# Kernel tuning notes

Measured on AMD Instinct MI355X. Metric: run time of the kernel, lower is better.

The kernel has to match this reference:

```python
import jax, jax.numpy as jnp
import numpy as np

D_MODEL, D_HEAD, N_HEAD, PERIOD = 1024, 64, 16, 30
B, T1, T2 = 2, 2048, 2048


def setup_inputs() -> dict:
    key = jax.random.key(0)
    ks = jax.random.split(key, 7)
    s_in = 1.0 / np.sqrt(D_MODEL)
    s_out = 1.0 / np.sqrt(N_HEAD * D_HEAD)
    return {
        "x": jax.random.normal(ks[0], (B, T1, D_MODEL), dtype=jnp.float32),
        "context": jax.random.normal(ks[1], (B, T2, D_MODEL), dtype=jnp.float32),
        "Wq": jax.random.uniform(ks[2], (N_HEAD * D_HEAD, D_MODEL), jnp.float32, -s_in, s_in),
        "Wk": jax.random.uniform(ks[3], (N_HEAD * D_HEAD, D_MODEL), jnp.float32, -s_in, s_in),
        "Wv": jax.random.uniform(ks[4], (N_HEAD * D_HEAD, D_MODEL), jnp.float32, -s_in, s_in),
        "Wo": jax.random.uniform(ks[5], (D_MODEL, N_HEAD * D_HEAD), jnp.float32, -s_out, s_out),
        "bo": jax.random.uniform(ks[6], (D_MODEL,), jnp.float32, -s_out, s_out),
    }


def reference(x, context, Wq, Wk, Wv, Wo, bo):
    Bx, T1x, _ = x.shape
    T2x = context.shape[1]
    scale = 1.0 / np.sqrt(D_HEAD).astype(np.float32)
    # projections (torch Linear: y = x @ W^T)
    q = (x @ Wq.T).reshape(Bx, T1x, N_HEAD, D_HEAD)
    k = (context @ Wk.T).reshape(Bx, T2x, N_HEAD, D_HEAD)
    v = (context @ Wv.T).reshape(Bx, T2x, N_HEAD, D_HEAD)
    # attention scores [B, H, T1, T2]
    scores = jnp.einsum('bihd,bjhd->bhij', q, k) * scale
    # ALiBi-style periodic distance bias
    dist = jnp.abs(jnp.arange(T1x)[:, None] - jnp.arange(T2x)[None, :])  # [T1,T2]
    bias = -(dist // PERIOD).astype(jnp.float32)                          # [T1,T2]
    head_scale = jnp.power(2.0, -jnp.arange(1, N_HEAD + 1, dtype=jnp.float32))
    biased = scores + bias[None, None, :, :] * head_scale[None, :, None, None]
    attn = jax.nn.softmax(biased, axis=-1)
    out = jnp.einsum('bhij,bjhd->bihd', attn, v).reshape(Bx, T1x, N_HEAD * D_HEAD)
    # output projection; dropout is identity in eval mode
    return out @ Wo.T + bo
```

## Files before the change

kernel.cpp:

```cpp
#include <hip/hip_runtime.h>
#include <hip/hip_fp16.h>

typedef _Float16 f16;
typedef __attribute__((ext_vector_type(8))) _Float16 f16x8;
typedef __attribute__((ext_vector_type(4))) _Float16 f16x4;
typedef __attribute__((ext_vector_type(2))) __fp16 fp16x2;
typedef __attribute__((ext_vector_type(4))) float f32x4;
typedef __attribute__((ext_vector_type(16))) float f32x16;

#define DM 1024
#define NH 16
#define DH 64
#define TT 2048
#define LOG2E 1.4426950408889634f
#define QSCALE 0.18033688f

__device__ __forceinline__ void gl16(const void* g, void* l) {
  __builtin_amdgcn_global_load_lds((const __attribute__((address_space(1))) void*)g,
                                   (__attribute__((address_space(3))) void*)l, 16, 0, 0);
}

#define SB0 __builtin_amdgcn_sched_barrier(0)

__global__ __launch_bounds__(256) void cvt_all(const float* __restrict__ x, const float* __restrict__ cx,
                                               const float* __restrict__ wq, const float* __restrict__ wk,
                                               const float* __restrict__ wv, const float* __restrict__ wo,
                                               f16* __restrict__ xb, f16* __restrict__ cb,
                                               f16* __restrict__ wqb, f16* __restrict__ wkb,
                                               f16* __restrict__ wvb, f16* __restrict__ wob,
                                               f16* __restrict__ FBf) {
  int idx = blockIdx.x * 256 + threadIdx.x;
  int stride = gridDim.x * 256;
  for (int i = idx; i < 3670016; i += stride) {
    if (i >= 3145728) {
      int c = i - 3145728;
      int half = c & 1, lane = (c >> 1) & 63, kvt = (c >> 7) & 63, qt = c >> 13;
      int qi = qt * 32 + (lane & 31);
      int jb = kvt * 32 + 16 * half + 8 * (lane >> 5);
      f16x8 v;
#pragma unroll
      for (int e = 0; e < 8; e++) {
        int d = qi - (jb + e); d = (d < 0) ? -d : d;
        v[e] = (f16)(d / 30);
      }
      reinterpret_cast<f16x8*>(FBf)[c] = v;
      continue;
    }
    const float* src; f16* dst; int off; float s = 1.0f;
    if (i < 2097152) {
      if (i < 1048576) { src = x; dst = xb; off = i; }
      else { src = cx; dst = cb; off = i - 1048576; }
    } else {
      int j = i - 2097152;
      int wsel = j >> 18;
      off = j & 262143;
      if (wsel == 0) { src = wq; dst = wqb; s = QSCALE; }
      else if (wsel == 1) { src = wk; dst = wkb; }
      else if (wsel == 2) { src = wv; dst = wvb; }
      else { src = wo; dst = wob; }
    }
    float4 v = reinterpret_cast<const float4*>(src)[off];
    f16x4 o = { (f16)(v.x * s), (f16)(v.y * s), (f16)(v.z * s), (f16)(v.w * s) };
    reinterpret_cast<f16x4*>(dst)[off] = o;
  }
}

__device__ __forceinline__ void gemm_mainloop(const f16* __restrict__ A, const f16* __restrict__ W,
                                              int bm, int bn, f16 (*As)[4096], f16 (*Bs)[4096],
                                              f32x4 (&acc)[4][4]) {
  int t = threadIdx.x;
  int w = t >> 6;
  int lane = t & 63, lr = lane & 15, g = lane >> 4;
  int wr = w >> 1, wc = w & 1;
  int scol = ((t & 3) ^ ((t >> 3) & 3)) * 8;
  const f16* a0 = A + (size_t)(bm + (t >> 2)) * DM + scol;
  const f16* b0 = W + (size_t)(bn + (t >> 2)) * DM + scol;
  int wo = w * 512;
  int szg = ((lr >> 1) & 3) << 4;

  auto STG = [&](int bufi, int kt) {
    gl16(a0 + kt, As[bufi] + wo);
    gl16(a0 + kt + (size_t)64 * DM, As[bufi] + 2048 + wo);
    gl16(b0 + kt, Bs[bufi] + wo);
    gl16(b0 + kt + (size_t)64 * DM, Bs[bufi] + 2048 + wo);
  };

  STG(0, 0);
  __syncthreads();
  int buf = 0;
  for (int kt = 0; kt < DM; kt += 32) {
    if (kt + 32 < DM) STG(buf ^ 1, kt + 32);
    const char* Ab = (const char*)As[buf];
    const char* Bb = (const char*)Bs[buf];
    f16x8 af[4], bf[4];
#pragma unroll
    for (int mi = 0; mi < 4; mi++) {
      int row = wr * 64 + mi * 16 + lr;
      af[mi] = *reinterpret_cast<const f16x8*>(Ab + row * 64 + ((g << 4) ^ szg));
    }
#pragma unroll
    for (int ni = 0; ni < 4; ni++) {
      int row = wc * 64 + ni * 16 + lr;
      bf[ni] = *reinterpret_cast<const f16x8*>(Bb + row * 64 + ((g << 4) ^ szg));
    }
    __builtin_amdgcn_s_setprio(1);
#pragma unroll
    for (int mi = 0; mi < 4; mi++)
#pragma unroll
      for (int ni = 0; ni < 4; ni++)
        acc[mi][ni] = __builtin_amdgcn_mfma_f32_16x16x32_f16(af[mi], bf[ni], acc[mi][ni], 0, 0, 0);
    __builtin_amdgcn_s_setprio(0);
    __syncthreads();
    buf ^= 1;
  }
}

__global__ __launch_bounds__(256) void qkv_gemm(const f16* __restrict__ xb, const f16* __restrict__ cb,
                                                const f16* __restrict__ wq, const f16* __restrict__ wk,
                                                const f16* __restrict__ wv,
                                                f16* __restrict__ Qo, f16* __restrict__ Ko,
                                                f16* __restrict__ Vt) {
  __shared__ f16 As[2][4096];
  __shared__ f16 Bs[2][4096];
  int gid = blockIdx.x >> 8;
  int bid = blockIdx.x & 255;
  int bm = (bid >> 3) * 128, bn = (bid & 7) * 128;
  const f16* A = (gid == 0) ? xb : cb;
  const f16* W = (gid == 0) ? wq : ((gid == 1) ? wk : wv);
  f32x4 acc[4][4] = {};
  gemm_mainloop(A, W, bm, bn, As, Bs, acc);

  int t = threadIdx.x, w = t >> 6, lane = t & 63, lr = lane & 15, g = lane >> 4;
  int wr = w >> 1, wc = w & 1;
  if (gid < 2) {
    f16* out = (gid == 0) ? Qo : Ko;
#pragma unroll
    for (int mi = 0; mi < 4; mi++) {
      int m0 = bm + wr * 64 + mi * 16 + 4 * g;
      int b = m0 >> 11, i0 = m0 & 2047;
#pragma unroll
      for (int ni = 0; ni < 4; ni++) {
        int n = bn + wc * 64 + ni * 16 + lr;
        int h = n >> 6, d = n & 63;
        size_t base = (((size_t)(b * NH + h)) * TT + i0) * DH + d;
#pragma unroll
        for (int r = 0; r < 4; r++)
          out[base + (size_t)r * DH] = (f16)acc[mi][ni][r];
      }
    }
  } else {
#pragma unroll
    for (int mi = 0; mi < 4; mi++) {
      int m0 = bm + wr * 64 + mi * 16 + 4 * g;
      int b = m0 >> 11, j0 = m0 & 2047;
#pragma unroll
      for (int ni = 0; ni < 4; ni++) {
        int n = bn + wc * 64 + ni * 16 + lr;
        int h = n >> 6, d = n & 63;
        f16x4 pk = { (f16)acc[mi][ni][0], (f16)acc[mi][ni][1],
                     (f16)acc[mi][ni][2], (f16)acc[mi][ni][3] };
        *reinterpret_cast<f16x4*>(&Vt[(((size_t)(b * NH + h)) * DH + d) * TT + j0]) = pk;
      }
    }
  }
}

__global__ __launch_bounds__(256) void out_gemm(const f16* __restrict__ Ob, const f16* __restrict__ wo,
                                                const float* __restrict__ bo, float* __restrict__ Y) {
  __shared__ f16 As[2][4096];
  __shared__ f16 Bs[2][4096];
  int bid = blockIdx.x;
  int bm = (bid >> 3) * 128, bn = (bid & 7) * 128;
  f32x4 acc[4][4] = {};
  gemm_mainloop(Ob, wo, bm, bn, As, Bs, acc);
  int t = threadIdx.x, w = t >> 6, lane = t & 63, lr = lane & 15, g = lane >> 4;
  int wr = w >> 1, wc = w & 1;
#pragma unroll
  for (int mi = 0; mi < 4; mi++) {
    int m0 = bm + wr * 64 + mi * 16 + 4 * g;
#pragma unroll
    for (int ni = 0; ni < 4; ni++) {
      int n = bn + wc * 64 + ni * 16 + lr;
      float bias = bo[n];
#pragma unroll
      for (int r = 0; r < 4; r++)
        Y[(size_t)(m0 + r) * DM + n] = acc[mi][ni][r] + bias;
    }
  }
}

__global__ __launch_bounds__(64, 2) void attn_kernel(const f16* __restrict__ Q, const f16* __restrict__ K,
                                                     const f16* __restrict__ V, const f16* __restrict__ FBf,
                                                     f16* __restrict__ O) {
  __shared__ f16 KV[2][4096];
  int o = blockIdx.x;
  int xcd = o & 7, idx = o >> 3;
  int bh = 4 * xcd + (idx >> 6), qt = idx & 63;
  int h = bh & 15, b = bh >> 4;
  int l = threadIdx.x;
  int col = l & 31, hi = l >> 5;
  int qi = qt * 32 + col;

  const f16* qp = Q + ((size_t)bh * TT + qi) * DH + hi * 8;
  f16x8 qf[4];
#pragma unroll
  for (int s = 0; s < 4; s++) qf[s] = *reinterpret_cast<const f16x8*>(qp + 16 * s);

  const float nc2 = -exp2f(-(float)(h + 1)) * LOG2E;
  const f16x8* fbp = reinterpret_cast<const f16x8*>(FBf) + ((size_t)qt << 13) + (l << 1);

  f32x4 rsv = { 0.f, 0.f, 0.f, 0.f };
  f32x16 oacc0 = {}, oacc1 = {};

  int r8 = l >> 3, G = l & 7;
  const f16 *kps[4], *vps[4];
#pragma unroll
  for (int c = 0; c < 4; c++) {
    int rho = c * 8 + r8;
    int g0k = G ^ (rho & 7);
    int J = (rho & 19) | ((rho & 4) << 1) | ((rho & 8) >> 1);
    kps[c] = K + ((size_t)bh * TT + J) * DH + g0k * 8;
    int pi = c * 8 + r8;
    int g0v = G ^ (pi & 7);
    int dv = 2 * pi + (g0v >> 2), jg = g0v & 3;
    vps[c] = V + ((size_t)bh * DH + dv) * TT + jg * 8;
  }

  auto STG = [&](int bufi, int kv0) {
    f16* base = KV[bufi];
#pragma unroll
    for (int c = 0; c < 4; c++) gl16(kps[c] + (size_t)kv0 * DH, base + c * 512);
#pragma unroll
    for (int c = 0; c < 4; c++) gl16(vps[c] + kv0, base + 2048 + c * 512);
  };

  int kbase = col * 128;
  int ksw[4];
#pragma unroll
  for (int s = 0; s < 4; s++) ksw[s] = ((2 * s + hi) ^ (col & 7)) << 4;
  int vbyte[2][2];
#pragma unroll
  for (int db = 0; db < 2; db++)
#pragma unroll
    for (int s2 = 0; s2 < 2; s2++) {
      int pi = 16 * db + (col >> 1);
      int gl = (col & 1) * 4 + 2 * s2 + hi;
      vbyte[db][s2] = 4096 + pi * 128 + ((gl ^ (pi & 7)) << 4);
    }

  auto CMP = [&](int bufi, f16x8 fb0, f16x8 fb1) {
    const char* Kb = (const char*)KV[bufi];
    f32x16 S = {};
    __builtin_amdgcn_s_setprio(1);
#pragma unroll
    for (int s = 0; s < 4; s++) {
      f16x8 ka = *reinterpret_cast<const f16x8*>(Kb + kbase + ksw[s]);
      S = __builtin_amdgcn_mfma_f32_32x32x16_f16(ka, qf[s], S, 0, 0, 0);
    }
    __builtin_amdgcn_s_setprio(0);
    float p[16];
#pragma unroll
    for (int r = 0; r < 16; r++) {
      float fbf = (float)((r < 8) ? fb0[r] : fb1[r - 8]);
      p[r] = __builtin_amdgcn_exp2f(fmaf(fbf, nc2, S[r]));
    }
#pragma unroll
    for (int r = 0; r < 4; r++) {
      f32x4 pv = { p[4 * r], p[4 * r + 1], p[4 * r + 2], p[4 * r + 3] };
      rsv += pv;
    }
    f16x8 pb[2];
#pragma unroll
    for (int s2 = 0; s2 < 2; s2++) {
      union { f16x8 v; fp16x2 hh[4]; } pu;
#pragma unroll
      for (int q2 = 0; q2 < 4; q2++)
        pu.hh[q2] = __builtin_amdgcn_cvt_pkrtz(p[8 * s2 + 2 * q2], p[8 * s2 + 2 * q2 + 1]);
      pb[s2] = pu.v;
    }
    __builtin_amdgcn_s_setprio(1);
#pragma unroll
    for (int s2 = 0; s2 < 2; s2++) {
      f16x8 va0 = *reinterpret_cast<const f16x8*>(Kb + vbyte[0][s2]);
      f16x8 va1 = *reinterpret_cast<const f16x8*>(Kb + vbyte[1][s2]);
      oacc0 = __builtin_amdgcn_mfma_f32_32x32x16_f16(va0, pb[s2], oacc0, 0, 0, 0);
      oacc1 = __builtin_amdgcn_mfma_f32_32x32x16_f16(va1, pb[s2], oacc1, 0, 0, 0);
    }
    __builtin_amdgcn_s_setprio(0);
  };

  STG(0, 0);
  f16x8 fA0 = fbp[0], fA1 = fbp[1];
  f16x8 fB0, fB1;

  for (int kvt = 0; kvt < 64; kvt += 2) {
    SB0;
    STG(1, (kvt + 1) << 5);
    fB0 = fbp[(kvt + 1) * 128];
    fB1 = fbp[(kvt + 1) * 128 + 1];
    asm volatile("s_waitcnt vmcnt(10)" ::: "memory");
    SB0;
    CMP(0, fA0, fA1);
    SB0;
    if (kvt + 2 < 64) {
      STG(0, (kvt + 2) << 5);
      fA0 = fbp[(kvt + 2) * 128];
      fA1 = fbp[(kvt + 2) * 128 + 1];
      asm volatile("s_waitcnt vmcnt(10)" ::: "memory");
    } else {
      asm volatile("s_waitcnt vmcnt(0)" ::: "memory");
    }
    SB0;
    CMP(1, fB0, fB1);
  }

  float lsum = (rsv[0] + rsv[1]) + (rsv[2] + rsv[3]);
  lsum += __shfl_xor(lsum, 32, 64);
  float inv = __builtin_amdgcn_rcpf(lsum);

  size_t ob = ((size_t)b * TT + qi) * DM + h * DH + 4 * hi;
  const f32x16* oa[2] = { &oacc0, &oacc1 };
#pragma unroll
  for (int db = 0; db < 2; db++)
#pragma unroll
    for (int a = 0; a < 4; a++) {
      f16x4 o4 = { (f16)((*oa[db])[4 * a] * inv),     (f16)((*oa[db])[4 * a + 1] * inv),
                   (f16)((*oa[db])[4 * a + 2] * inv), (f16)((*oa[db])[4 * a + 3] * inv) };
      *reinterpret_cast<f16x4*>(&O[ob + 32 * db + 8 * a]) = o4;
    }
}

extern "C" void kernel_launch(void* const* d_in, const int* in_sizes, int n_in,
                              void* d_out, int out_size, void* d_ws, size_t ws_size,
                              hipStream_t stream) {
  const float* x  = (const float*)d_in[0];
  const float* cx = (const float*)d_in[1];
  const float* Wq = (const float*)d_in[2];
  const float* Wk = (const float*)d_in[3];
  const float* Wv = (const float*)d_in[4];
  const float* Wo = (const float*)d_in[5];
  const float* bo = (const float*)d_in[6];
  float* Y = (float*)d_out;

  const size_t NTOK = (size_t)2 * TT;
  f16* p = (f16*)d_ws;
  f16* xb  = p; p += NTOK * DM;
  f16* cb  = p; p += NTOK * DM;
  f16* wqb = p; p += (size_t)DM * DM;
  f16* wkb = p; p += (size_t)DM * DM;
  f16* wvb = p; p += (size_t)DM * DM;
  f16* wob = p; p += (size_t)DM * DM;
  f16* Qb  = p; p += NTOK * DM;
  f16* Kb  = p; p += NTOK * DM;
  f16* Vtb = p; p += NTOK * DM;
  f16* Ob  = p; p += NTOK * DM;
  f16* FBt = p;

  cvt_all<<<2048, 256, 0, stream>>>(x, cx, Wq, Wk, Wv, Wo, xb, cb, wqb, wkb, wvb, wob, FBt);
  qkv_gemm<<<768, 256, 0, stream>>>(xb, cb, wqb, wkb, wvb, Qb, Kb, Vtb);
  attn_kernel<<<2048, 64, 0, stream>>>(Qb, Kb, Vtb, FBt, Ob);
  out_gemm<<<256, 256, 0, stream>>>(Ob, wob, bo, Y);
}
```

Baseline: 144.1 us.

## Share K/V tiles across four waves per block with register-staged double buffering

The attention kernel moves from one 64-thread wave per 32 queries to a 256-thread block of four waves covering 128 queries. The four waves share each K/V tile staged in LDS, and each tile is now 64 keys instead of 32. Staging changes from direct global-to-LDS loads to register loads followed by LDS writes, with block barriers between buffers. This cuts redundant K/V global traffic by a factor of four, at the cost of barrier synchronisation and higher register pressure from doubled score tiles.

```diff
diff --git a/kernel.cpp b/kernel.cpp
--- a/kernel.cpp
+++ b/kernel.cpp
@@ -21,6 +21,7 @@
 }
 
 #define SB0 __builtin_amdgcn_sched_barrier(0)
+#define LGKM0 asm volatile("s_waitcnt lgkmcnt(0)" ::: "memory")
 
 __global__ __launch_bounds__(256) void cvt_all(const float* __restrict__ x, const float* __restrict__ cx,
                                                const float* __restrict__ wq, const float* __restrict__ wk,
@@ -189,17 +190,19 @@
   }
 }
 
-__global__ __launch_bounds__(64, 2) void attn_kernel(const f16* __restrict__ Q, const f16* __restrict__ K,
-                                                     const f16* __restrict__ V, const f16* __restrict__ FBf,
-                                                     f16* __restrict__ O) {
-  __shared__ f16 KV[2][4096];
+struct FB4 { f16x8 a, b, c, d; };
+
+__global__ __launch_bounds__(256, 2) void attn_kernel(const f16* __restrict__ Q, const f16* __restrict__ K,
+                                                      const f16* __restrict__ V, const f16* __restrict__ FBf,
+                                                      f16* __restrict__ O) {
+  __shared__ f16 KV[2][8192];
   int o = blockIdx.x;
   int xcd = o & 7, idx = o >> 3;
-  int bh = 4 * xcd + (idx >> 6), qt = idx & 63;
+  int bh = 4 * xcd + (idx >> 4), qblk = idx & 15;
   int h = bh & 15, b = bh >> 4;
-  int l = threadIdx.x;
-  int col = l & 31, hi = l >> 5;
-  int qi = qt * 32 + col;
+  int tt = threadIdx.x, w = tt >> 6, lane = tt & 63;
+  int col = lane & 31, hi = lane >> 5;
+  int qi = qblk * 128 + w * 32 + col;
 
   const f16* qp = Q + ((size_t)bh * TT + qi) * DH + hi * 8;
   f16x8 qf[4];
@@ -207,111 +210,124 @@
   for (int s = 0; s < 4; s++) qf[s] = *reinterpret_cast<const f16x8*>(qp + 16 * s);
 
   const float nc2 = -exp2f(-(float)(h + 1)) * LOG2E;
-  const f16x8* fbp = reinterpret_cast<const f16x8*>(FBf) + ((size_t)qt << 13) + (l << 1);
+  int qtp = qblk * 4 + w;
+  const f16x8* fbp = reinterpret_cast<const f16x8*>(FBf) + ((size_t)qtp << 13) + (lane << 1);
 
   f32x4 rsv = { 0.f, 0.f, 0.f, 0.f };
   f32x16 oacc0 = {}, oacc1 = {};
 
-  int r8 = l >> 3, G = l & 7;
-  const f16 *kps[4], *vps[4];
-#pragma unroll
-  for (int c = 0; c < 4; c++) {
-    int rho = c * 8 + r8;
-    int g0k = G ^ (rho & 7);
-    int J = (rho & 19) | ((rho & 4) << 1) | ((rho & 8) >> 1);
-    kps[c] = K + ((size_t)bh * TT + J) * DH + g0k * 8;
-    int pi = c * 8 + r8;
-    int g0v = G ^ (pi & 7);
-    int dv = 2 * pi + (g0v >> 2), jg = g0v & 3;
-    vps[c] = V + ((size_t)bh * DH + dv) * TT + jg * 8;
-  }
-
-  auto STG = [&](int bufi, int kv0) {
-    f16* base = KV[bufi];
-#pragma unroll
-    for (int c = 0; c < 4; c++) gl16(kps[c] + (size_t)kv0 * DH, base + c * 512);
-#pragma unroll
-    for (int c = 0; c < 4; c++) gl16(vps[c] + kv0, base + 2048 + c * 512);
-  };
-
-  int kbase = col * 128;
+  int rho0 = tt >> 3, G = tt & 7;
+  int f0 = (rho0 & 7) ^ (3 * ((rho0 >> 4) & 1));
+  int J0 = (rho0 & 19) | ((rho0 & 4) << 1) | ((rho0 & 8) >> 1);
+  const f16* kp0 = K + ((size_t)bh * TT + J0) * DH + (G ^ f0) * 8;
+  const f16* kp1 = K + ((size_t)bh * TT + 32 + J0) * DH + (G ^ f0) * 8;
+  const f16* vp0 = V + ((size_t)bh * DH + rho0) * TT + (G ^ f0) * 8;
+  const f16* vp1 = V + ((size_t)bh * DH + 32 + rho0) * TT + (G ^ f0) * 8;
+
+  f16x8 r0, r1, r2, r3;
+  auto LOADR = [&](int kv0) {
+    r0 = *reinterpret_cast<const f16x8*>(kp0 + (size_t)kv0 * DH);
+    r1 = *reinterpret_cast<const f16x8*>(kp1 + (size_t)kv0 * DH);
+    r2 = *reinterpret_cast<const f16x8*>(vp0 + kv0);
+    r3 = *reinterpret_cast<const f16x8*>(vp1 + kv0);
+  };
+  auto WRITE = [&](int bufi) {
+    char* base = (char*)KV[bufi];
+    *reinterpret_cast<f16x8*>(base + tt * 16) = r0;
+    *reinterpret_cast<f16x8*>(base + 4096 + tt * 16) = r1;
+    *reinterpret_cast<f16x8*>(base + 8192 + tt * 16) = r2;
+    *reinterpret_cast<f16x8*>(base + 12288 + tt * 16) = r3;
+  };
+
+  int fcol = (col & 7) ^ (3 * ((col >> 4) & 1));
+  int kb0 = col * 128;
   int ksw[4];
 #pragma unroll
-  for (int s = 0; s < 4; s++) ksw[s] = ((2 * s + hi) ^ (col & 7)) << 4;
-  int vbyte[2][2];
-#pragma unroll
-  for (int db = 0; db < 2; db++)
+  for (int s = 0; s < 4; s++) ksw[s] = ((2 * s + hi) ^ fcol) << 4;
+
+  auto FBLOAD = [&](int t) {
+    FB4 f;
+    f.a = fbp[256 * t];
+    f.b = fbp[256 * t + 1];
+    f.c = fbp[256 * t + 128];
+    f.d = fbp[256 * t + 129];
+    return f;
+  };
+
+  auto CMP = [&](int bufi, const FB4& fb) {
+    const char* Kb = (const char*)KV[bufi];
+    f32x16 S0 = {}, S1 = {};
+    __builtin_amdgcn_s_setprio(1);
+#pragma unroll
+    for (int s = 0; s < 4; s++) {
+      f16x8 ka0 = *reinterpret_cast<const f16x8*>(Kb + kb0 + ksw[s]);
+      f16x8 ka1 = *reinterpret_cast<const f16x8*>(Kb + 4096 + kb0 + ksw[s]);
+      S0 = __builtin_amdgcn_mfma_f32_32x32x16_f16(ka0, qf[s], S0, 0, 0, 0);
+      S1 = __builtin_amdgcn_mfma_f32_32x32x16_f16(ka1, qf[s], S1, 0, 0, 0);
+    }
+    __builtin_amdgcn_s_setprio(0);
+    float p0[16], p1[16];
+#pragma unroll
+    for (int r = 0; r < 16; r++) {
+      float fb0 = (float)((r < 8) ? fb.a[r] : fb.b[r - 8]);
+      float fb1 = (float)((r < 8) ? fb.c[r] : fb.d[r - 8]);
+      p0[r] = __builtin_amdgcn_exp2f(fmaf(fb0, nc2, S0[r]));
+      p1[r] = __builtin_amdgcn_exp2f(fmaf(fb1, nc2, S1[r]));
+    }
+#pragma unroll
+    for (int r = 0; r < 4; r++) {
+      f32x4 pa = { p0[4 * r], p0[4 * r + 1], p0[4 * r + 2], p0[4 * r + 3] };
+      f32x4 pc = { p1[4 * r], p1[4 * r + 1], p1[4 * r + 2], p1[4 * r + 3] };
+      rsv += pa + pc;
+    }
+    f16x8 pb[4];
 #pragma unroll
     for (int s2 = 0; s2 < 2; s2++) {
-      int pi = 16 * db + (col >> 1);
-      int gl = (col & 1) * 4 + 2 * s2 + hi;
-      vbyte[db][s2] = 4096 + pi * 128 + ((gl ^ (pi & 7)) << 4);
-    }
-
-  auto CMP = [&](int bufi, f16x8 fb0, f16x8 fb1) {
-    const char* Kb = (const char*)KV[bufi];
-    f32x16 S = {};
+      union { f16x8 v; fp16x2 hh[4]; } u0, u1;
+#pragma unroll
+      for (int q2 = 0; q2 < 4; q2++) {
+        u0.hh[q2] = __builtin_amdgcn_cvt_pkrtz(p0[8 * s2 + 2 * q2], p0[8 * s2 + 2 * q2 + 1]);
+        u1.hh[q2] = __builtin_amdgcn_cvt_pkrtz(p1[8 * s2 + 2 * q2], p1[8 * s2 + 2 * q2 + 1]);
+      }
+      pb[s2] = u0.v; pb[2 + s2] = u1.v;
+    }
     __builtin_amdgcn_s_setprio(1);
 #pragma unroll
-    for (int s = 0; s < 4; s++) {
-      f16x8 ka = *reinterpret_cast<const f16x8*>(Kb + kbase + ksw[s]);
-      S = __builtin_amdgcn_mfma_f32_32x32x16_f16(ka, qf[s], S, 0, 0, 0);
-    }
-    __builtin_amdgcn_s_setprio(0);
-    float p[16];
-#pragma unroll
-    for (int r = 0; r < 16; r++) {
-      float fbf = (float)((r < 8) ? fb0[r] : fb1[r - 8]);
-      p[r] = __builtin_amdgcn_exp2f(fmaf(fbf, nc2, S[r]));
-    }
-#pragma unroll
-    for (int r = 0; r < 4; r++) {
-      f32x4 pv = { p[4 * r], p[4 * r + 1], p[4 * r + 2], p[4 * r + 3] };
-      rsv += pv;
-    }
-    f16x8 pb[2];
-#pragma unroll
-    for (int s2 = 0; s2 < 2; s2++) {
-      union { f16x8 v; fp16x2 hh[4]; } pu;
-#pragma unroll
-      for (int q2 = 0; q2 < 4; q2++)
-        pu.hh[q2] = __builtin_amdgcn_cvt_pkrtz(p[8 * s2 + 2 * q2], p[8 * s2 + 2 * q2 + 1]);
-      pb[s2] = pu.v;
-    }
-    __builtin_amdgcn_s_setprio(1);
-#pragma unroll
-    for (int s2 = 0; s2 < 2; s2++) {
-      f16x8 va0 = *reinterpret_cast<const f16x8*>(Kb + vbyte[0][s2]);
-      f16x8 va1 = *reinterpret_cast<const f16x8*>(Kb + vbyte[1][s2]);
+    for (int s2 = 0; s2 < 4; s2++) {
+      f16x8 va0 = *reinterpret_cast<const f16x8*>(Kb + 8192 + kb0 + ksw[s2]);
+      f16x8 va1 = *reinterpret_cast<const f16x8*>(Kb + 12288 + kb0 + ksw[s2]);
       oacc0 = __builtin_amdgcn_mfma_f32_32x32x16_f16(va0, pb[s2], oacc0, 0, 0, 0);
       oacc1 = __builtin_amdgcn_mfma_f32_32x32x16_f16(va1, pb[s2], oacc1, 0, 0, 0);
     }
     __builtin_amdgcn_s_setprio(0);
   };
 
-  STG(0, 0);
-  f16x8 fA0 = fbp[0], fA1 = fbp[1];
-  f16x8 fB0, fB1;
-
-  for (int kvt = 0; kvt < 64; kvt += 2) {
+  LOADR(0);
+  WRITE(0);
+  LOADR(64);
+  FB4 fA = FBLOAD(0);
+  FB4 fB = FBLOAD(1);
+  LGKM0;
+  __builtin_amdgcn_s_barrier();
+  SB0;
+
+#pragma unroll 1
+  for (int tp = 0; tp < 16; tp++) {
+    int t0 = 2 * tp;
+    CMP(0, fA);
+    WRITE(1);
+    if (t0 + 2 < 32) { LOADR((t0 + 2) << 6); fA = FBLOAD(t0 + 2); }
+    LGKM0;
+    __builtin_amdgcn_s_barrier();
     SB0;
-    STG(1, (kvt + 1) << 5);
-    fB0 = fbp[(kvt + 1) * 128];
-    fB1 = fbp[(kvt + 1) * 128 + 1];
-    asm volatile("s_waitcnt vmcnt(10)" ::: "memory");
-    SB0;
-    CMP(0, fA0, fA1);
-    SB0;
-    if (kvt + 2 < 64) {
-      STG(0, (kvt + 2) << 5);
-      fA0 = fbp[(kvt + 2) * 128];
-      fA1 = fbp[(kvt + 2) * 128 + 1];
-      asm volatile("s_waitcnt vmcnt(10)" ::: "memory");
-    } else {
-      asm volatile("s_waitcnt vmcnt(0)" ::: "memory");
-    }
-    SB0;
-    CMP(1, fB0, fB1);
+    CMP(1, fB);
+    if (t0 + 2 < 32) {
+      WRITE(0);
+      if (t0 + 3 < 32) { LOADR((t0 + 3) << 6); fB = FBLOAD(t0 + 3); }
+      LGKM0;
+      __builtin_amdgcn_s_barrier();
+      SB0;
+    }
   }
 
   float lsum = (rsv[0] + rsv[1]) + (rsv[2] + rsv[3]);
@@ -358,6 +374,6 @@
 
   cvt_all<<<2048, 256, 0, stream>>>(x, cx, Wq, Wk, Wv, Wo, xb, cb, wqb, wkb, wvb, wob, FBt);
   qkv_gemm<<<768, 256, 0, stream>>>(xb, cb, wqb, wkb, wvb, Qb, Kb, Vtb);
-  attn_kernel<<<2048, 64, 0, stream>>>(Qb, Kb, Vtb, FBt, Ob);
+  attn_kernel<<<512, 256, 0, stream>>>(Qb, Kb, Vtb, FBt, Ob);
   out_gemm<<<256, 256, 0, stream>>>(Ob, wob, bo, Y);
 }
```

New measurement: 127.2 us. -11.7%, faster.
